# Optimization experiments

Measured on AMD Instinct MI355X. Metric: run time of the kernel, lower is better.

Reference implementation:

```python
import jax, jax.numpy as jnp
import numpy as np

LOG2 = float(np.log(2.0))
NEG_INF = float('-inf')


def log1mexp(x):
    # numerically accurate log(1 - exp(x)) for x < 0
    return jnp.where(x > -LOG2, jnp.log(-jnp.expm1(x)), jnp.log1p(-jnp.exp(x)))


def encode_input_log(pos):
    neg = log1mexp(pos)
    # interleave [pos_i, neg_i] then prepend constants [-inf (log 0), 0 (log 1)]
    result = jnp.stack([pos, neg], axis=1).reshape(-1)
    constants = jnp.array([NEG_INF, 0.0], dtype=pos.dtype)
    return jnp.concatenate([constants, result])


def sum_layer(x, ptrs, csr, n):
    # product node in log semiring: segment-sum of gathered log-values
    return jax.ops.segment_sum(x[ptrs], csr, num_segments=n)


def logsum_layer(x, ptrs, csr, n, epsilon=1e-15):
    # sum node in log semiring: numerically stable segment log-sum-exp
    g = x[ptrs]
    m = jax.lax.stop_gradient(jax.ops.segment_max(g, csr, num_segments=n))
    z = g - m[csr]
    z = jnp.nan_to_num(z, nan=0.0, posinf=jnp.inf, neginf=-jnp.inf)  # (-inf)-(-inf) -> 0
    s = jax.ops.segment_sum(jnp.exp(z), csr, num_segments=n) + epsilon
    return jnp.log(s) + m


def setup_inputs() -> dict:
    key = jax.random.key(0)
    n_vars = 2_000_000
    deg = 4
    Ns = [4_000_000, 2_000_000, 1_000_000, 500_000]
    sizes_in = [2 + 2 * n_vars] + Ns[:-1]
    ks = jax.random.split(key, 1 + len(Ns))
    # log-probabilities strictly in (log eps, log(1-eps)) so log1mexp is finite
    u = jax.random.uniform(ks[0], (n_vars,), dtype=jnp.float32, minval=1e-6, maxval=1.0 - 1e-6)
    inp = {"weights": jnp.log(u)}
    for i, n in enumerate(Ns):
        e = n * deg
        inp[f"ptrs{i}"] = jax.random.randint(ks[i + 1], (e,), 0, sizes_in[i], dtype=jnp.int32)
        inp[f"csr{i}"] = jnp.repeat(jnp.arange(n, dtype=jnp.int32), deg)  # unrolled CSR, fan-in=deg
        inp[f"n{i}"] = n
    return inp


def reference(weights, ptrs0, csr0, ptrs1, csr1, ptrs2, csr2, ptrs3, csr3, n0, n1, n2, n3):
    x = encode_input_log(weights)
    x = sum_layer(x, ptrs0, csr0, n0)      # layer 0: product (even)
    x = logsum_layer(x, ptrs1, csr1, n1)   # layer 1: sum (odd)
    x = sum_layer(x, ptrs2, csr2, n2)      # layer 2: product
    x = logsum_layer(x, ptrs3, csr3, n3)   # layer 3: sum
    return x
```

## Files before the change

kernel.cpp:

```cpp
#include <hip/hip_runtime.h>
#include <math.h>

#define NEG_INF (-INFINITY)

typedef int      v4i __attribute__((ext_vector_type(4)));
typedef float    v4f __attribute__((ext_vector_type(4)));
typedef _Float16 v4h __attribute__((ext_vector_type(4)));

__device__ __forceinline__ float fast_log1mexp(float v) {
    if (v > -0.125f) {
        float e = v * (1.0f + v * (0.5f + v * (0.16666667f + v * 0.041666667f)));
        return __logf(-e);
    }
    return __logf(1.0f - __expf(v));
}

__global__ __launch_bounds__(256) void cvt_kernel(const float* __restrict__ w,
                                                  _Float16* __restrict__ wh, int n) {
    int i = blockIdx.x * blockDim.x + threadIdx.x;
    int n4 = n >> 2;
    if (i < n4) {
        v4f v = reinterpret_cast<const v4f*>(w)[i];
        v4h o;
        o.x = (_Float16)v.x; o.y = (_Float16)v.y;
        o.z = (_Float16)v.z; o.w = (_Float16)v.w;
        reinterpret_cast<v4h*>(wh)[i] = o;
    }
    int base = n4 << 2;
    if (i < (n - base)) wh[base + i] = (_Float16)w[base + i];
}

__device__ __forceinline__ int widx(int p) { int j = (p >> 1) - 1; return j < 0 ? 0 : j; }
__device__ __forceinline__ float fixw(int p, float v) {
    float r = (p & 1) ? fast_log1mexp(v) : v;
    if (p < 2) r = (p == 0) ? NEG_INF : 0.0f;
    return r;
}

__global__ __launch_bounds__(256) void sum4_enc_kernel(const _Float16* __restrict__ wh,
                                                       const v4i* __restrict__ ptrs,
                                                       _Float16* __restrict__ y, int n, int h) {
    int t = blockIdx.x * blockDim.x + threadIdx.x;
    if (t >= h) return;
    int i0 = t, i1 = t + h, i2 = t + 2 * h, i3 = t + 3 * h;
    int c1 = i1 < n ? i1 : 0, c2 = i2 < n ? i2 : 0, c3 = i3 < n ? i3 : 0;
    v4i p0 = __builtin_nontemporal_load(ptrs + i0);
    v4i p1 = __builtin_nontemporal_load(ptrs + c1);
    v4i p2 = __builtin_nontemporal_load(ptrs + c2);
    v4i p3 = __builtin_nontemporal_load(ptrs + c3);
    float g00 = (float)wh[widx(p0.x)], g01 = (float)wh[widx(p0.y)];
    float g02 = (float)wh[widx(p0.z)], g03 = (float)wh[widx(p0.w)];
    float g10 = (float)wh[widx(p1.x)], g11 = (float)wh[widx(p1.y)];
    float g12 = (float)wh[widx(p1.z)], g13 = (float)wh[widx(p1.w)];
    float g20 = (float)wh[widx(p2.x)], g21 = (float)wh[widx(p2.y)];
    float g22 = (float)wh[widx(p2.z)], g23 = (float)wh[widx(p2.w)];
    float g30 = (float)wh[widx(p3.x)], g31 = (float)wh[widx(p3.y)];
    float g32 = (float)wh[widx(p3.z)], g33 = (float)wh[widx(p3.w)];
    float s0 = (fixw(p0.x, g00) + fixw(p0.y, g01)) + (fixw(p0.z, g02) + fixw(p0.w, g03));
    float s1 = (fixw(p1.x, g10) + fixw(p1.y, g11)) + (fixw(p1.z, g12) + fixw(p1.w, g13));
    float s2 = (fixw(p2.x, g20) + fixw(p2.y, g21)) + (fixw(p2.z, g22) + fixw(p2.w, g23));
    float s3 = (fixw(p3.x, g30) + fixw(p3.y, g31)) + (fixw(p3.z, g32) + fixw(p3.w, g33));
    __builtin_nontemporal_store((_Float16)s0, y + i0);
    if (i1 < n) __builtin_nontemporal_store((_Float16)s1, y + i1);
    if (i2 < n) __builtin_nontemporal_store((_Float16)s2, y + i2);
    if (i3 < n) __builtin_nontemporal_store((_Float16)s3, y + i3);
}

__global__ __launch_bounds__(256) void sum4_h2h_kernel(const _Float16* __restrict__ x,
                                                       const v4i* __restrict__ ptrs,
                                                       _Float16* __restrict__ y, int n, int h) {
    int t = blockIdx.x * blockDim.x + threadIdx.x;
    if (t >= h) return;
    int i0 = t, i1 = t + h, i2 = t + 2 * h, i3 = t + 3 * h;
    int c1 = i1 < n ? i1 : 0, c2 = i2 < n ? i2 : 0, c3 = i3 < n ? i3 : 0;
    v4i p0 = __builtin_nontemporal_load(ptrs + i0);
    v4i p1 = __builtin_nontemporal_load(ptrs + c1);
    v4i p2 = __builtin_nontemporal_load(ptrs + c2);
    v4i p3 = __builtin_nontemporal_load(ptrs + c3);
    float s0 = ((float)x[p0.x] + (float)x[p0.y]) + ((float)x[p0.z] + (float)x[p0.w]);
    float s1 = ((float)x[p1.x] + (float)x[p1.y]) + ((float)x[p1.z] + (float)x[p1.w]);
    float s2 = ((float)x[p2.x] + (float)x[p2.y]) + ((float)x[p2.z] + (float)x[p2.w]);
    float s3 = ((float)x[p3.x] + (float)x[p3.y]) + ((float)x[p3.z] + (float)x[p3.w]);
    __builtin_nontemporal_store((_Float16)s0, y + i0);
    if (i1 < n) __builtin_nontemporal_store((_Float16)s1, y + i1);
    if (i2 < n) __builtin_nontemporal_store((_Float16)s2, y + i2);
    if (i3 < n) __builtin_nontemporal_store((_Float16)s3, y + i3);
}

__device__ __forceinline__ float lse4(float a, float b, float c, float d) {
    float m = fmaxf(fmaxf(a, b), fmaxf(c, d));
    if (m == NEG_INF) return NEG_INF;
    float s = __expf(a - m) + __expf(b - m) + __expf(c - m) + __expf(d - m) + 1e-15f;
    return __logf(s) + m;
}

__global__ __launch_bounds__(256) void logsum4_h2h_kernel(const _Float16* __restrict__ x,
                                                          const v4i* __restrict__ ptrs,
                                                          _Float16* __restrict__ y, int n, int h) {
    int t = blockIdx.x * blockDim.x + threadIdx.x;
    if (t >= h) return;
    int i0 = t, i1 = t + h, i2 = t + 2 * h, i3 = t + 3 * h;
    int c1 = i1 < n ? i1 : 0, c2 = i2 < n ? i2 : 0, c3 = i3 < n ? i3 : 0;
    v4i p0 = __builtin_nontemporal_load(ptrs + i0);
    v4i p1 = __builtin_nontemporal_load(ptrs + c1);
    v4i p2 = __builtin_nontemporal_load(ptrs + c2);
    v4i p3 = __builtin_nontemporal_load(ptrs + c3);
    float a0 = (float)x[p0.x], b0 = (float)x[p0.y], e0 = (float)x[p0.z], d0 = (float)x[p0.w];
    float a1 = (float)x[p1.x], b1 = (float)x[p1.y], e1 = (float)x[p1.z], d1 = (float)x[p1.w];
    float a2 = (float)x[p2.x], b2 = (float)x[p2.y], e2 = (float)x[p2.z], d2 = (float)x[p2.w];
    float a3 = (float)x[p3.x], b3 = (float)x[p3.y], e3 = (float)x[p3.z], d3 = (float)x[p3.w];
    float s0 = lse4(a0, b0, e0, d0);
    float s1 = lse4(a1, b1, e1, d1);
    float s2 = lse4(a2, b2, e2, d2);
    float s3 = lse4(a3, b3, e3, d3);
    __builtin_nontemporal_store((_Float16)s0, y + i0);
    if (i1 < n) __builtin_nontemporal_store((_Float16)s1, y + i1);
    if (i2 < n) __builtin_nontemporal_store((_Float16)s2, y + i2);
    if (i3 < n) __builtin_nontemporal_store((_Float16)s3, y + i3);
}

__global__ __launch_bounds__(256) void logsum4_h2f_kernel(const _Float16* __restrict__ x,
                                                          const v4i* __restrict__ ptrs,
                                                          float* __restrict__ y, int n, int h) {
    int t = blockIdx.x * blockDim.x + threadIdx.x;
    if (t >= h) return;
    int i0 = t, i1 = t + h, i2 = t + 2 * h, i3 = t + 3 * h;
    int c1 = i1 < n ? i1 : 0, c2 = i2 < n ? i2 : 0, c3 = i3 < n ? i3 : 0;
    v4i p0 = __builtin_nontemporal_load(ptrs + i0);
    v4i p1 = __builtin_nontemporal_load(ptrs + c1);
    v4i p2 = __builtin_nontemporal_load(ptrs + c2);
    v4i p3 = __builtin_nontemporal_load(ptrs + c3);
    float a0 = (float)x[p0.x], b0 = (float)x[p0.y], e0 = (float)x[p0.z], d0 = (float)x[p0.w];
    float a1 = (float)x[p1.x], b1 = (float)x[p1.y], e1 = (float)x[p1.z], d1 = (float)x[p1.w];
    float a2 = (float)x[p2.x], b2 = (float)x[p2.y], e2 = (float)x[p2.z], d2 = (float)x[p2.w];
    float a3 = (float)x[p3.x], b3 = (float)x[p3.y], e3 = (float)x[p3.z], d3 = (float)x[p3.w];
    float s0 = lse4(a0, b0, e0, d0);
    float s1 = lse4(a1, b1, e1, d1);
    float s2 = lse4(a2, b2, e2, d2);
    float s3 = lse4(a3, b3, e3, d3);
    __builtin_nontemporal_store(s0, y + i0);
    if (i1 < n) __builtin_nontemporal_store(s1, y + i1);
    if (i2 < n) __builtin_nontemporal_store(s2, y + i2);
    if (i3 < n) __builtin_nontemporal_store(s3, y + i3);
}

extern "C" void kernel_launch(void* const* d_in, const int* in_sizes, int n_in,
                              void* d_out, int out_size, void* d_ws, size_t ws_size,
                              hipStream_t stream) {
    const float* w     = (const float*)d_in[0];
    const v4i*   ptrs0 = (const v4i*)d_in[1];
    const v4i*   ptrs1 = (const v4i*)d_in[4];
    const v4i*   ptrs2 = (const v4i*)d_in[7];
    const v4i*   ptrs3 = (const v4i*)d_in[10];

    const int n_vars = in_sizes[0];
    const int n0 = in_sizes[1] / 4;
    const int n1 = in_sizes[4] / 4;
    const int n2 = in_sizes[7] / 4;
    const int n3 = in_sizes[10] / 4;

    char* ws = (char*)d_ws;
    size_t off = 0;
    _Float16* wh = (_Float16*)(ws + off); off += ((size_t)n_vars * 2 + 255) & ~(size_t)255;
    _Float16* y0 = (_Float16*)(ws + off); off += ((size_t)n0 * 2 + 255) & ~(size_t)255;
    _Float16* y1 = (_Float16*)(ws + off); off += ((size_t)n1 * 2 + 255) & ~(size_t)255;
    _Float16* y2 = (_Float16*)(ws + off);
    float* out = (float*)d_out;

    const int B = 256;
    int hc = (n_vars + 3) / 4;
    int h0 = (n0 + 3) / 4, h1 = (n1 + 3) / 4, h2 = (n2 + 3) / 4, h3 = (n3 + 3) / 4;

    cvt_kernel        <<<(hc + B - 1) / B, B, 0, stream>>>(w, wh, n_vars);
    sum4_enc_kernel   <<<(h0 + B - 1) / B, B, 0, stream>>>(wh, ptrs0, y0, n0, h0);
    logsum4_h2h_kernel<<<(h1 + B - 1) / B, B, 0, stream>>>(y0, ptrs1, y1, n1, h1);
    sum4_h2h_kernel   <<<(h2 + B - 1) / B, B, 0, stream>>>(y1, ptrs2, y2, n2, h2);
    logsum4_h2f_kernel<<<(h3 + B - 1) / B, B, 0, stream>>>(y2, ptrs3, out, n3, h3);
}
```

Measured before the change: 373.0 us.

## Fuse all layers into one cooperative persistent kernel with grid syncs

Replaces the five separate kernel launches with a single cooperative persistent kernel that grid-strides over each layer and uses grid.sync between stages. It also turns the intermediate fp16 stores into normal (temporal) stores so the next layer's gathers may hit in cache. The aim is to remove launch gaps and tail effects between layers. In exchange it adds grid-wide barrier costs, a host-side device-property and occupancy query on every call, and a grid capped at 2048 blocks, which may reduce memory-level parallelism for these gather-bound layers.

Result: slower. 888.0 us (+138.1%).

```diff
diff --git a/kernel.cpp b/kernel.cpp
--- a/kernel.cpp
+++ b/kernel.cpp
@@ -1,5 +1,8 @@
 #include <hip/hip_runtime.h>
+#include <hip/hip_cooperative_groups.h>
 #include <math.h>
+
+namespace cg = cooperative_groups;
 
 #define NEG_INF (-INFINITY)
 
@@ -15,76 +18,11 @@
     return __logf(1.0f - __expf(v));
 }
 
-__global__ __launch_bounds__(256) void cvt_kernel(const float* __restrict__ w,
-                                                  _Float16* __restrict__ wh, int n) {
-    int i = blockIdx.x * blockDim.x + threadIdx.x;
-    int n4 = n >> 2;
-    if (i < n4) {
-        v4f v = reinterpret_cast<const v4f*>(w)[i];
-        v4h o;
-        o.x = (_Float16)v.x; o.y = (_Float16)v.y;
-        o.z = (_Float16)v.z; o.w = (_Float16)v.w;
-        reinterpret_cast<v4h*>(wh)[i] = o;
-    }
-    int base = n4 << 2;
-    if (i < (n - base)) wh[base + i] = (_Float16)w[base + i];
-}
-
 __device__ __forceinline__ int widx(int p) { int j = (p >> 1) - 1; return j < 0 ? 0 : j; }
 __device__ __forceinline__ float fixw(int p, float v) {
     float r = (p & 1) ? fast_log1mexp(v) : v;
     if (p < 2) r = (p == 0) ? NEG_INF : 0.0f;
     return r;
-}
-
-__global__ __launch_bounds__(256) void sum4_enc_kernel(const _Float16* __restrict__ wh,
-                                                       const v4i* __restrict__ ptrs,
-                                                       _Float16* __restrict__ y, int n, int h) {
-    int t = blockIdx.x * blockDim.x + threadIdx.x;
-    if (t >= h) return;
-    int i0 = t, i1 = t + h, i2 = t + 2 * h, i3 = t + 3 * h;
-    int c1 = i1 < n ? i1 : 0, c2 = i2 < n ? i2 : 0, c3 = i3 < n ? i3 : 0;
-    v4i p0 = __builtin_nontemporal_load(ptrs + i0);
-    v4i p1 = __builtin_nontemporal_load(ptrs + c1);
-    v4i p2 = __builtin_nontemporal_load(ptrs + c2);
-    v4i p3 = __builtin_nontemporal_load(ptrs + c3);
-    float g00 = (float)wh[widx(p0.x)], g01 = (float)wh[widx(p0.y)];
-    float g02 = (float)wh[widx(p0.z)], g03 = (float)wh[widx(p0.w)];
-    float g10 = (float)wh[widx(p1.x)], g11 = (float)wh[widx(p1.y)];
-    float g12 = (float)wh[widx(p1.z)], g13 = (float)wh[widx(p1.w)];
-    float g20 = (float)wh[widx(p2.x)], g21 = (float)wh[widx(p2.y)];
-    float g22 = (float)wh[widx(p2.z)], g23 = (float)wh[widx(p2.w)];
-    float g30 = (float)wh[widx(p3.x)], g31 = (float)wh[widx(p3.y)];
-    float g32 = (float)wh[widx(p3.z)], g33 = (float)wh[widx(p3.w)];
-    float s0 = (fixw(p0.x, g00) + fixw(p0.y, g01)) + (fixw(p0.z, g02) + fixw(p0.w, g03));
-    float s1 = (fixw(p1.x, g10) + fixw(p1.y, g11)) + (fixw(p1.z, g12) + fixw(p1.w, g13));
-    float s2 = (fixw(p2.x, g20) + fixw(p2.y, g21)) + (fixw(p2.z, g22) + fixw(p2.w, g23));
-    float s3 = (fixw(p3.x, g30) + fixw(p3.y, g31)) + (fixw(p3.z, g32) + fixw(p3.w, g33));
-    __builtin_nontemporal_store((_Float16)s0, y + i0);
-    if (i1 < n) __builtin_nontemporal_store((_Float16)s1, y + i1);
-    if (i2 < n) __builtin_nontemporal_store((_Float16)s2, y + i2);
-    if (i3 < n) __builtin_nontemporal_store((_Float16)s3, y + i3);
-}
-
-__global__ __launch_bounds__(256) void sum4_h2h_kernel(const _Float16* __restrict__ x,
-                                                       const v4i* __restrict__ ptrs,
-                                                       _Float16* __restrict__ y, int n, int h) {
-    int t = blockIdx.x * blockDim.x + threadIdx.x;
-    if (t >= h) return;
-    int i0 = t, i1 = t + h, i2 = t + 2 * h, i3 = t + 3 * h;
-    int c1 = i1 < n ? i1 : 0, c2 = i2 < n ? i2 : 0, c3 = i3 < n ? i3 : 0;
-    v4i p0 = __builtin_nontemporal_load(ptrs + i0);
-    v4i p1 = __builtin_nontemporal_load(ptrs + c1);
-    v4i p2 = __builtin_nontemporal_load(ptrs + c2);
-    v4i p3 = __builtin_nontemporal_load(ptrs + c3);
-    float s0 = ((float)x[p0.x] + (float)x[p0.y]) + ((float)x[p0.z] + (float)x[p0.w]);
-    float s1 = ((float)x[p1.x] + (float)x[p1.y]) + ((float)x[p1.z] + (float)x[p1.w]);
-    float s2 = ((float)x[p2.x] + (float)x[p2.y]) + ((float)x[p2.z] + (float)x[p2.w]);
-    float s3 = ((float)x[p3.x] + (float)x[p3.y]) + ((float)x[p3.z] + (float)x[p3.w]);
-    __builtin_nontemporal_store((_Float16)s0, y + i0);
-    if (i1 < n) __builtin_nontemporal_store((_Float16)s1, y + i1);
-    if (i2 < n) __builtin_nontemporal_store((_Float16)s2, y + i2);
-    if (i3 < n) __builtin_nontemporal_store((_Float16)s3, y + i3);
 }
 
 __device__ __forceinline__ float lse4(float a, float b, float c, float d) {
@@ -94,54 +32,117 @@
     return __logf(s) + m;
 }
 
-__global__ __launch_bounds__(256) void logsum4_h2h_kernel(const _Float16* __restrict__ x,
-                                                          const v4i* __restrict__ ptrs,
-                                                          _Float16* __restrict__ y, int n, int h) {
-    int t = blockIdx.x * blockDim.x + threadIdx.x;
-    if (t >= h) return;
-    int i0 = t, i1 = t + h, i2 = t + 2 * h, i3 = t + 3 * h;
-    int c1 = i1 < n ? i1 : 0, c2 = i2 < n ? i2 : 0, c3 = i3 < n ? i3 : 0;
-    v4i p0 = __builtin_nontemporal_load(ptrs + i0);
-    v4i p1 = __builtin_nontemporal_load(ptrs + c1);
-    v4i p2 = __builtin_nontemporal_load(ptrs + c2);
-    v4i p3 = __builtin_nontemporal_load(ptrs + c3);
-    float a0 = (float)x[p0.x], b0 = (float)x[p0.y], e0 = (float)x[p0.z], d0 = (float)x[p0.w];
-    float a1 = (float)x[p1.x], b1 = (float)x[p1.y], e1 = (float)x[p1.z], d1 = (float)x[p1.w];
-    float a2 = (float)x[p2.x], b2 = (float)x[p2.y], e2 = (float)x[p2.z], d2 = (float)x[p2.w];
-    float a3 = (float)x[p3.x], b3 = (float)x[p3.y], e3 = (float)x[p3.z], d3 = (float)x[p3.w];
-    float s0 = lse4(a0, b0, e0, d0);
-    float s1 = lse4(a1, b1, e1, d1);
-    float s2 = lse4(a2, b2, e2, d2);
-    float s3 = lse4(a3, b3, e3, d3);
-    __builtin_nontemporal_store((_Float16)s0, y + i0);
-    if (i1 < n) __builtin_nontemporal_store((_Float16)s1, y + i1);
-    if (i2 < n) __builtin_nontemporal_store((_Float16)s2, y + i2);
-    if (i3 < n) __builtin_nontemporal_store((_Float16)s3, y + i3);
-}
+__global__ void __launch_bounds__(256, 8)
+fused_kernel(const float* __restrict__ w,
+             const v4i* __restrict__ ptrs0, const v4i* __restrict__ ptrs1,
+             const v4i* __restrict__ ptrs2, const v4i* __restrict__ ptrs3,
+             _Float16* __restrict__ wh, _Float16* __restrict__ y0,
+             _Float16* __restrict__ y1, _Float16* __restrict__ y2,
+             float* __restrict__ out,
+             int n_vars, int n0, int n1, int n2, int n3) {
+    cg::grid_group grid = cg::this_grid();
+    const int T = gridDim.x * blockDim.x;
+    const int t = blockIdx.x * blockDim.x + threadIdx.x;
 
-__global__ __launch_bounds__(256) void logsum4_h2f_kernel(const _Float16* __restrict__ x,
-                                                          const v4i* __restrict__ ptrs,
-                                                          float* __restrict__ y, int n, int h) {
-    int t = blockIdx.x * blockDim.x + threadIdx.x;
-    if (t >= h) return;
-    int i0 = t, i1 = t + h, i2 = t + 2 * h, i3 = t + 3 * h;
-    int c1 = i1 < n ? i1 : 0, c2 = i2 < n ? i2 : 0, c3 = i3 < n ? i3 : 0;
-    v4i p0 = __builtin_nontemporal_load(ptrs + i0);
-    v4i p1 = __builtin_nontemporal_load(ptrs + c1);
-    v4i p2 = __builtin_nontemporal_load(ptrs + c2);
-    v4i p3 = __builtin_nontemporal_load(ptrs + c3);
-    float a0 = (float)x[p0.x], b0 = (float)x[p0.y], e0 = (float)x[p0.z], d0 = (float)x[p0.w];
-    float a1 = (float)x[p1.x], b1 = (float)x[p1.y], e1 = (float)x[p1.z], d1 = (float)x[p1.w];
-    float a2 = (float)x[p2.x], b2 = (float)x[p2.y], e2 = (float)x[p2.z], d2 = (float)x[p2.w];
-    float a3 = (float)x[p3.x], b3 = (float)x[p3.y], e3 = (float)x[p3.z], d3 = (float)x[p3.w];
-    float s0 = lse4(a0, b0, e0, d0);
-    float s1 = lse4(a1, b1, e1, d1);
-    float s2 = lse4(a2, b2, e2, d2);
-    float s3 = lse4(a3, b3, e3, d3);
-    __builtin_nontemporal_store(s0, y + i0);
-    if (i1 < n) __builtin_nontemporal_store(s1, y + i1);
-    if (i2 < n) __builtin_nontemporal_store(s2, y + i2);
-    if (i3 < n) __builtin_nontemporal_store(s3, y + i3);
+    int n4 = n_vars >> 2;
+    for (int i = t; i < n4; i += T) {
+        v4f v = reinterpret_cast<const v4f*>(w)[i];
+        v4h o;
+        o.x = (_Float16)v.x; o.y = (_Float16)v.y;
+        o.z = (_Float16)v.z; o.w = (_Float16)v.w;
+        reinterpret_cast<v4h*>(wh)[i] = o;
+    }
+    for (int i = (n4 << 2) + t; i < n_vars; i += T) wh[i] = (_Float16)w[i];
+    grid.sync();
+
+    for (int base = t; base < n0; base += 4 * T) {
+        int i0 = base, i1 = base + T, i2 = base + 2 * T, i3 = base + 3 * T;
+        int c1 = i1 < n0 ? i1 : 0, c2 = i2 < n0 ? i2 : 0, c3 = i3 < n0 ? i3 : 0;
+        v4i p0 = __builtin_nontemporal_load(ptrs0 + i0);
+        v4i p1 = __builtin_nontemporal_load(ptrs0 + c1);
+        v4i p2 = __builtin_nontemporal_load(ptrs0 + c2);
+        v4i p3 = __builtin_nontemporal_load(ptrs0 + c3);
+        float g00 = (float)wh[widx(p0.x)], g01 = (float)wh[widx(p0.y)];
+        float g02 = (float)wh[widx(p0.z)], g03 = (float)wh[widx(p0.w)];
+        float g10 = (float)wh[widx(p1.x)], g11 = (float)wh[widx(p1.y)];
+        float g12 = (float)wh[widx(p1.z)], g13 = (float)wh[widx(p1.w)];
+        float g20 = (float)wh[widx(p2.x)], g21 = (float)wh[widx(p2.y)];
+        float g22 = (float)wh[widx(p2.z)], g23 = (float)wh[widx(p2.w)];
+        float g30 = (float)wh[widx(p3.x)], g31 = (float)wh[widx(p3.y)];
+        float g32 = (float)wh[widx(p3.z)], g33 = (float)wh[widx(p3.w)];
+        float s0 = (fixw(p0.x, g00) + fixw(p0.y, g01)) + (fixw(p0.z, g02) + fixw(p0.w, g03));
+        float s1 = (fixw(p1.x, g10) + fixw(p1.y, g11)) + (fixw(p1.z, g12) + fixw(p1.w, g13));
+        float s2 = (fixw(p2.x, g20) + fixw(p2.y, g21)) + (fixw(p2.z, g22) + fixw(p2.w, g23));
+        float s3 = (fixw(p3.x, g30) + fixw(p3.y, g31)) + (fixw(p3.z, g32) + fixw(p3.w, g33));
+        y0[i0] = (_Float16)s0;
+        if (i1 < n0) y0[i1] = (_Float16)s1;
+        if (i2 < n0) y0[i2] = (_Float16)s2;
+        if (i3 < n0) y0[i3] = (_Float16)s3;
+    }
+    grid.sync();
+
+    for (int base = t; base < n1; base += 4 * T) {
+        int i0 = base, i1 = base + T, i2 = base + 2 * T, i3 = base + 3 * T;
+        int c1 = i1 < n1 ? i1 : 0, c2 = i2 < n1 ? i2 : 0, c3 = i3 < n1 ? i3 : 0;
+        v4i p0 = __builtin_nontemporal_load(ptrs1 + i0);
+        v4i p1 = __builtin_nontemporal_load(ptrs1 + c1);
+        v4i p2 = __builtin_nontemporal_load(ptrs1 + c2);
+        v4i p3 = __builtin_nontemporal_load(ptrs1 + c3);
+        float a0 = (float)y0[p0.x], b0 = (float)y0[p0.y], e0 = (float)y0[p0.z], d0 = (float)y0[p0.w];
+        float a1 = (float)y0[p1.x], b1 = (float)y0[p1.y], e1 = (float)y0[p1.z], d1 = (float)y0[p1.w];
+        float a2 = (float)y0[p2.x], b2 = (float)y0[p2.y], e2 = (float)y0[p2.z], d2 = (float)y0[p2.w];
+        float a3 = (float)y0[p3.x], b3 = (float)y0[p3.y], e3 = (float)y0[p3.z], d3 = (float)y0[p3.w];
+        float s0 = lse4(a0, b0, e0, d0);
+        float s1 = lse4(a1, b1, e1, d1);
+        float s2 = lse4(a2, b2, e2, d2);
+        float s3 = lse4(a3, b3, e3, d3);
+        y1[i0] = (_Float16)s0;
+        if (i1 < n1) y1[i1] = (_Float16)s1;
+        if (i2 < n1) y1[i2] = (_Float16)s2;
+        if (i3 < n1) y1[i3] = (_Float16)s3;
+    }
+    grid.sync();
+
+    for (int base = t; base < n2; base += 4 * T) {
+        int i0 = base, i1 = base + T, i2 = base + 2 * T, i3 = base + 3 * T;
+        int c0 = i0 < n2 ? i0 : 0;
+        int c1 = i1 < n2 ? i1 : 0, c2 = i2 < n2 ? i2 : 0, c3 = i3 < n2 ? i3 : 0;
+        v4i p0 = __builtin_nontemporal_load(ptrs2 + c0);
+        v4i p1 = __builtin_nontemporal_load(ptrs2 + c1);
+        v4i p2 = __builtin_nontemporal_load(ptrs2 + c2);
+        v4i p3 = __builtin_nontemporal_load(ptrs2 + c3);
+        float s0 = ((float)y1[p0.x] + (float)y1[p0.y]) + ((float)y1[p0.z] + (float)y1[p0.w]);
+        float s1 = ((float)y1[p1.x] + (float)y1[p1.y]) + ((float)y1[p1.z] + (float)y1[p1.w]);
+        float s2 = ((float)y1[p2.x] + (float)y1[p2.y]) + ((float)y1[p2.z] + (float)y1[p2.w]);
+        float s3 = ((float)y1[p3.x] + (float)y1[p3.y]) + ((float)y1[p3.z] + (float)y1[p3.w]);
+        if (i0 < n2) y2[i0] = (_Float16)s0;
+        if (i1 < n2) y2[i1] = (_Float16)s1;
+        if (i2 < n2) y2[i2] = (_Float16)s2;
+        if (i3 < n2) y2[i3] = (_Float16)s3;
+    }
+    grid.sync();
+
+    for (int base = t; base < n3; base += 4 * T) {
+        int i0 = base, i1 = base + T, i2 = base + 2 * T, i3 = base + 3 * T;
+        int c0 = i0 < n3 ? i0 : 0;
+        int c1 = i1 < n3 ? i1 : 0, c2 = i2 < n3 ? i2 : 0, c3 = i3 < n3 ? i3 : 0;
+        v4i p0 = __builtin_nontemporal_load(ptrs3 + c0);
+        v4i p1 = __builtin_nontemporal_load(ptrs3 + c1);
+        v4i p2 = __builtin_nontemporal_load(ptrs3 + c2);
+        v4i p3 = __builtin_nontemporal_load(ptrs3 + c3);
+        float a0 = (float)y2[p0.x], b0 = (float)y2[p0.y], e0 = (float)y2[p0.z], d0 = (float)y2[p0.w];
+        float a1 = (float)y2[p1.x], b1 = (float)y2[p1.y], e1 = (float)y2[p1.z], d1 = (float)y2[p1.w];
+        float a2 = (float)y2[p2.x], b2 = (float)y2[p2.y], e2 = (float)y2[p2.z], d2 = (float)y2[p2.w];
+        float a3 = (float)y2[p3.x], b3 = (float)y2[p3.y], e3 = (float)y2[p3.z], d3 = (float)y2[p3.w];
+        float s0 = lse4(a0, b0, e0, d0);
+        float s1 = lse4(a1, b1, e1, d1);
+        float s2 = lse4(a2, b2, e2, d2);
+        float s3 = lse4(a3, b3, e3, d3);
+        if (i0 < n3) __builtin_nontemporal_store(s0, out + i0);
+        if (i1 < n3) __builtin_nontemporal_store(s1, out + i1);
+        if (i2 < n3) __builtin_nontemporal_store(s2, out + i2);
+        if (i3 < n3) __builtin_nontemporal_store(s3, out + i3);
+    }
 }
 
 extern "C" void kernel_launch(void* const* d_in, const int* in_sizes, int n_in,
@@ -153,11 +154,11 @@
     const v4i*   ptrs2 = (const v4i*)d_in[7];
     const v4i*   ptrs3 = (const v4i*)d_in[10];
 
-    const int n_vars = in_sizes[0];
-    const int n0 = in_sizes[1] / 4;
-    const int n1 = in_sizes[4] / 4;
-    const int n2 = in_sizes[7] / 4;
-    const int n3 = in_sizes[10] / 4;
+    int n_vars = in_sizes[0];
+    int n0 = in_sizes[1] / 4;
+    int n1 = in_sizes[4] / 4;
+    int n2 = in_sizes[7] / 4;
+    int n3 = in_sizes[10] / 4;
 
     char* ws = (char*)d_ws;
     size_t off = 0;
@@ -167,13 +168,16 @@
     _Float16* y2 = (_Float16*)(ws + off);
     float* out = (float*)d_out;
 
-    const int B = 256;
-    int hc = (n_vars + 3) / 4;
-    int h0 = (n0 + 3) / 4, h1 = (n1 + 3) / 4, h2 = (n2 + 3) / 4, h3 = (n3 + 3) / 4;
+    hipDeviceProp_t prop;
+    hipGetDeviceProperties(&prop, 0);
+    int bpcu = 0;
+    hipOccupancyMaxActiveBlocksPerMultiprocessor(&bpcu, (const void*)fused_kernel, 256, 0);
+    if (bpcu < 1) bpcu = 1;
+    int grid = prop.multiProcessorCount * bpcu;
+    if (grid > 2048) grid = 2048;
 
-    cvt_kernel        <<<(hc + B - 1) / B, B, 0, stream>>>(w, wh, n_vars);
-    sum4_enc_kernel   <<<(h0 + B - 1) / B, B, 0, stream>>>(wh, ptrs0, y0, n0, h0);
-    logsum4_h2h_kernel<<<(h1 + B - 1) / B, B, 0, stream>>>(y0, ptrs1, y1, n1, h1);
-    sum4_h2h_kernel   <<<(h2 + B - 1) / B, B, 0, stream>>>(y1, ptrs2, y2, n2, h2);
-    logsum4_h2f_kernel<<<(h3 + B - 1) / B, B, 0, stream>>>(y2, ptrs3, out, n3, h3);
+    void* args[] = { (void*)&w, (void*)&ptrs0, (void*)&ptrs1, (void*)&ptrs2, (void*)&ptrs3,
+                     (void*)&wh, (void*)&y0, (void*)&y1, (void*)&y2, (void*)&out,
+                     (void*)&n_vars, (void*)&n0, (void*)&n1, (void*)&n2, (void*)&n3 };
+    hipLaunchCooperativeKernel((const void*)fused_kernel, dim3(grid), dim3(256), args, 0, stream);
 }
```

## Split layer-1 logsum gather into two passes by source index half

Applied to the files above, without the earlier changes.

The layer-1 log-sum-exp kernel is replaced by two passes. Each pass gathers only the pointers that fall in one half of the 4M-entry fp16 input, so that half (about 4 MB) can stay cache-resident during random gathers. The first pass writes a partial LSE to a scratch buffer and the second merges it with the other half's partial. This costs reading the pointer array twice, an extra launch, and a scratch write and read, in exchange for better locality on the random gathers.

After: 357.0 us. 1.04x faster.

```diff
diff --git a/kernel.cpp b/kernel.cpp
--- a/kernel.cpp
+++ b/kernel.cpp
@@ -66,6 +66,109 @@
     if (i3 < n) __builtin_nontemporal_store((_Float16)s3, y + i3);
 }
 
+__device__ __forceinline__ float plse4(float a, float b, float c, float d) {
+    float m = fmaxf(fmaxf(a, b), fmaxf(c, d));
+    if (m == NEG_INF) return NEG_INF;
+    float s = __expf(a - m) + __expf(b - m) + __expf(c - m) + __expf(d - m);
+    return __logf(s) + m;
+}
+
+__global__ __launch_bounds__(256) void l1a_kernel(const _Float16* __restrict__ x,
+                                                  const v4i* __restrict__ ptrs,
+                                                  _Float16* __restrict__ LA,
+                                                  int n, int h, int half) {
+    int t = blockIdx.x * blockDim.x + threadIdx.x;
+    if (t >= h) return;
+    int i0 = t, i1 = t + h, i2 = t + 2 * h, i3 = t + 3 * h;
+    int c1 = i1 < n ? i1 : 0, c2 = i2 < n ? i2 : 0, c3 = i3 < n ? i3 : 0;
+    v4i p0 = __builtin_nontemporal_load(ptrs + i0);
+    v4i p1 = __builtin_nontemporal_load(ptrs + c1);
+    v4i p2 = __builtin_nontemporal_load(ptrs + c2);
+    v4i p3 = __builtin_nontemporal_load(ptrs + c3);
+    float a0 = NEG_INF, b0 = NEG_INF, e0 = NEG_INF, d0 = NEG_INF;
+    float a1 = NEG_INF, b1 = NEG_INF, e1 = NEG_INF, d1 = NEG_INF;
+    float a2 = NEG_INF, b2 = NEG_INF, e2 = NEG_INF, d2 = NEG_INF;
+    float a3 = NEG_INF, b3 = NEG_INF, e3 = NEG_INF, d3 = NEG_INF;
+    if (p0.x < half) a0 = (float)x[p0.x];
+    if (p0.y < half) b0 = (float)x[p0.y];
+    if (p0.z < half) e0 = (float)x[p0.z];
+    if (p0.w < half) d0 = (float)x[p0.w];
+    if (p1.x < half) a1 = (float)x[p1.x];
+    if (p1.y < half) b1 = (float)x[p1.y];
+    if (p1.z < half) e1 = (float)x[p1.z];
+    if (p1.w < half) d1 = (float)x[p1.w];
+    if (p2.x < half) a2 = (float)x[p2.x];
+    if (p2.y < half) b2 = (float)x[p2.y];
+    if (p2.z < half) e2 = (float)x[p2.z];
+    if (p2.w < half) d2 = (float)x[p2.w];
+    if (p3.x < half) a3 = (float)x[p3.x];
+    if (p3.y < half) b3 = (float)x[p3.y];
+    if (p3.z < half) e3 = (float)x[p3.z];
+    if (p3.w < half) d3 = (float)x[p3.w];
+    float s0 = plse4(a0, b0, e0, d0);
+    float s1 = plse4(a1, b1, e1, d1);
+    float s2 = plse4(a2, b2, e2, d2);
+    float s3 = plse4(a3, b3, e3, d3);
+    __builtin_nontemporal_store((_Float16)s0, LA + i0);
+    if (i1 < n) __builtin_nontemporal_store((_Float16)s1, LA + i1);
+    if (i2 < n) __builtin_nontemporal_store((_Float16)s2, LA + i2);
+    if (i3 < n) __builtin_nontemporal_store((_Float16)s3, LA + i3);
+}
+
+__device__ __forceinline__ float merge_lse(float LA, float LB) {
+    float m = fmaxf(LA, LB);
+    if (m == NEG_INF) return NEG_INF;
+    float s = __expf(LA - m) + __expf(LB - m) + 1e-15f;
+    return __logf(s) + m;
+}
+
+__global__ __launch_bounds__(256) void l1b_kernel(const _Float16* __restrict__ x,
+                                                  const v4i* __restrict__ ptrs,
+                                                  const _Float16* __restrict__ LA,
+                                                  _Float16* __restrict__ y,
+                                                  int n, int h, int half) {
+    int t = blockIdx.x * blockDim.x + threadIdx.x;
+    if (t >= h) return;
+    int i0 = t, i1 = t + h, i2 = t + 2 * h, i3 = t + 3 * h;
+    int c1 = i1 < n ? i1 : 0, c2 = i2 < n ? i2 : 0, c3 = i3 < n ? i3 : 0;
+    v4i p0 = __builtin_nontemporal_load(ptrs + i0);
+    v4i p1 = __builtin_nontemporal_load(ptrs + c1);
+    v4i p2 = __builtin_nontemporal_load(ptrs + c2);
+    v4i p3 = __builtin_nontemporal_load(ptrs + c3);
+    float la0 = (float)__builtin_nontemporal_load(LA + i0);
+    float la1 = (float)__builtin_nontemporal_load(LA + c1);
+    float la2 = (float)__builtin_nontemporal_load(LA + c2);
+    float la3 = (float)__builtin_nontemporal_load(LA + c3);
+    float a0 = NEG_INF, b0 = NEG_INF, e0 = NEG_INF, d0 = NEG_INF;
+    float a1 = NEG_INF, b1 = NEG_INF, e1 = NEG_INF, d1 = NEG_INF;
+    float a2 = NEG_INF, b2 = NEG_INF, e2 = NEG_INF, d2 = NEG_INF;
+    float a3 = NEG_INF, b3 = NEG_INF, e3 = NEG_INF, d3 = NEG_INF;
+    if (p0.x >= half) a0 = (float)x[p0.x];
+    if (p0.y >= half) b0 = (float)x[p0.y];
+    if (p0.z >= half) e0 = (float)x[p0.z];
+    if (p0.w >= half) d0 = (float)x[p0.w];
+    if (p1.x >= half) a1 = (float)x[p1.x];
+    if (p1.y >= half) b1 = (float)x[p1.y];
+    if (p1.z >= half) e1 = (float)x[p1.z];
+    if (p1.w >= half) d1 = (float)x[p1.w];
+    if (p2.x >= half) a2 = (float)x[p2.x];
+    if (p2.y >= half) b2 = (float)x[p2.y];
+    if (p2.z >= half) e2 = (float)x[p2.z];
+    if (p2.w >= half) d2 = (float)x[p2.w];
+    if (p3.x >= half) a3 = (float)x[p3.x];
+    if (p3.y >= half) b3 = (float)x[p3.y];
+    if (p3.z >= half) e3 = (float)x[p3.z];
+    if (p3.w >= half) d3 = (float)x[p3.w];
+    float s0 = merge_lse(la0, plse4(a0, b0, e0, d0));
+    float s1 = merge_lse(la1, plse4(a1, b1, e1, d1));
+    float s2 = merge_lse(la2, plse4(a2, b2, e2, d2));
+    float s3 = merge_lse(la3, plse4(a3, b3, e3, d3));
+    __builtin_nontemporal_store((_Float16)s0, y + i0);
+    if (i1 < n) __builtin_nontemporal_store((_Float16)s1, y + i1);
+    if (i2 < n) __builtin_nontemporal_store((_Float16)s2, y + i2);
+    if (i3 < n) __builtin_nontemporal_store((_Float16)s3, y + i3);
+}
+
 __global__ __launch_bounds__(256) void sum4_h2h_kernel(const _Float16* __restrict__ x,
                                                        const v4i* __restrict__ ptrs,
                                                        _Float16* __restrict__ y, int n, int h) {
@@ -92,31 +195,6 @@
     if (m == NEG_INF) return NEG_INF;
     float s = __expf(a - m) + __expf(b - m) + __expf(c - m) + __expf(d - m) + 1e-15f;
     return __logf(s) + m;
-}
-
-__global__ __launch_bounds__(256) void logsum4_h2h_kernel(const _Float16* __restrict__ x,
-                                                          const v4i* __restrict__ ptrs,
-                                                          _Float16* __restrict__ y, int n, int h) {
-    int t = blockIdx.x * blockDim.x + threadIdx.x;
-    if (t >= h) return;
-    int i0 = t, i1 = t + h, i2 = t + 2 * h, i3 = t + 3 * h;
-    int c1 = i1 < n ? i1 : 0, c2 = i2 < n ? i2 : 0, c3 = i3 < n ? i3 : 0;
-    v4i p0 = __builtin_nontemporal_load(ptrs + i0);
-    v4i p1 = __builtin_nontemporal_load(ptrs + c1);
-    v4i p2 = __builtin_nontemporal_load(ptrs + c2);
-    v4i p3 = __builtin_nontemporal_load(ptrs + c3);
-    float a0 = (float)x[p0.x], b0 = (float)x[p0.y], e0 = (float)x[p0.z], d0 = (float)x[p0.w];
-    float a1 = (float)x[p1.x], b1 = (float)x[p1.y], e1 = (float)x[p1.z], d1 = (float)x[p1.w];
-    float a2 = (float)x[p2.x], b2 = (float)x[p2.y], e2 = (float)x[p2.z], d2 = (float)x[p2.w];
-    float a3 = (float)x[p3.x], b3 = (float)x[p3.y], e3 = (float)x[p3.z], d3 = (float)x[p3.w];
-    float s0 = lse4(a0, b0, e0, d0);
-    float s1 = lse4(a1, b1, e1, d1);
-    float s2 = lse4(a2, b2, e2, d2);
-    float s3 = lse4(a3, b3, e3, d3);
-    __builtin_nontemporal_store((_Float16)s0, y + i0);
-    if (i1 < n) __builtin_nontemporal_store((_Float16)s1, y + i1);
-    if (i2 < n) __builtin_nontemporal_store((_Float16)s2, y + i2);
-    if (i3 < n) __builtin_nontemporal_store((_Float16)s3, y + i3);
 }
 
 __global__ __launch_bounds__(256) void logsum4_h2f_kernel(const _Float16* __restrict__ x,
@@ -164,16 +242,19 @@
     _Float16* wh = (_Float16*)(ws + off); off += ((size_t)n_vars * 2 + 255) & ~(size_t)255;
     _Float16* y0 = (_Float16*)(ws + off); off += ((size_t)n0 * 2 + 255) & ~(size_t)255;
     _Float16* y1 = (_Float16*)(ws + off); off += ((size_t)n1 * 2 + 255) & ~(size_t)255;
-    _Float16* y2 = (_Float16*)(ws + off);
+    _Float16* y2 = (_Float16*)(ws + off); off += ((size_t)n2 * 2 + 255) & ~(size_t)255;
+    _Float16* LA = (_Float16*)(ws + off);
     float* out = (float*)d_out;
 
     const int B = 256;
     int hc = (n_vars + 3) / 4;
     int h0 = (n0 + 3) / 4, h1 = (n1 + 3) / 4, h2 = (n2 + 3) / 4, h3 = (n3 + 3) / 4;
+    int half0 = n0 / 2;
 
     cvt_kernel        <<<(hc + B - 1) / B, B, 0, stream>>>(w, wh, n_vars);
     sum4_enc_kernel   <<<(h0 + B - 1) / B, B, 0, stream>>>(wh, ptrs0, y0, n0, h0);
-    logsum4_h2h_kernel<<<(h1 + B - 1) / B, B, 0, stream>>>(y0, ptrs1, y1, n1, h1);
+    l1a_kernel        <<<(h1 + B - 1) / B, B, 0, stream>>>(y0, ptrs1, LA, n1, h1, half0);
+    l1b_kernel        <<<(h1 + B - 1) / B, B, 0, stream>>>(y0, ptrs1, LA, y1, n1, h1, half0);
     sum4_h2h_kernel   <<<(h2 + B - 1) / B, B, 0, stream>>>(y1, ptrs2, y2, n2, h2);
     logsum4_h2f_kernel<<<(h3 + B - 1) / B, B, 0, stream>>>(y2, ptrs3, out, n3, h3);
 }
```
